# Optimization experiments

Measured on AMD Instinct MI355X. Metric: run time of the kernel, lower is better.

Reference implementation:

```python
import jax, jax.numpy as jnp
import numpy as np

N, E, C, D, H = 50000, 1600000, 50000, 128, 512


def setup_inputs() -> dict:
    key = jax.random.key(0)
    ks = jax.random.split(key, 16)
    s = jnp.float32(0.02)  # keep activations stable through 3 layers
    inp = {}
    inp["x"] = jax.random.normal(ks[0], (N, D), jnp.float32)
    inp["edge_index"] = jax.random.randint(ks[1], (2, E), 0, N)
    inp["first_edge"] = jax.random.randint(ks[2], (2,), 0, N)
    inp["candidate_edges"] = jax.random.randint(ks[3], (C, 2), 0, N)
    inp["t"] = jax.random.uniform(ks[4], (1, 1), jnp.float32)
    dims = [(D, H), (H, H), (H, H)]
    i = 5
    for l, (di, do) in enumerate(dims):
        inp[f"gin{l}_w1"] = jax.random.normal(ks[i], (di, do), jnp.float32) * s; i += 1
        inp[f"gin{l}_b1"] = jnp.zeros((do,), jnp.float32)
        inp[f"gin{l}_w2"] = jax.random.normal(ks[i], (do, do), jnp.float32) * s; i += 1
        inp[f"gin{l}_b2"] = jnp.zeros((do,), jnp.float32)
    inp["pred_w1"] = jax.random.normal(ks[i], (5 * H, H), jnp.float32) * s; i += 1
    inp["pred_b1"] = jnp.zeros((H,), jnp.float32)
    inp["pred_w2"] = jax.random.normal(ks[i], (H, 1), jnp.float32) * s; i += 1
    inp["pred_b2"] = jnp.zeros((1,), jnp.float32)
    inp["time_w1"] = jax.random.normal(ks[i], (1, H), jnp.float32) * s; i += 1
    inp["time_b1"] = jnp.zeros((H,), jnp.float32)
    inp["time_w2"] = jax.random.normal(ks[i], (H, H), jnp.float32) * s; i += 1
    inp["time_b2"] = jnp.zeros((H,), jnp.float32)
    return inp


def _edge_rep(x, u, v):
    # 'sum_absdiff': cat([x_u + x_v, |x_u - x_v|]) -> 2*H features
    xu, xv = x[u], x[v]
    return jnp.concatenate([xu + xv, jnp.abs(xu - xv)], axis=-1)


def reference(x, edge_index, first_edge, candidate_edges, t,
              gin0_w1, gin0_b1, gin0_w2, gin0_b2,
              gin1_w1, gin1_b1, gin1_w2, gin1_b2,
              gin2_w1, gin2_b1, gin2_w2, gin2_b2,
              pred_w1, pred_b1, pred_w2, pred_b2,
              time_w1, time_b1, time_w2, time_b2):
    src, dst = edge_index[0], edge_index[1]
    layers = [(gin0_w1, gin0_b1, gin0_w2, gin0_b2),
              (gin1_w1, gin1_b1, gin1_w2, gin1_b2),
              (gin2_w1, gin2_b1, gin2_w2, gin2_b2)]
    # GINConv (eps=0): h_i = MLP(x_i + sum_{j->i} x_j)
    for w1, b1, w2, b2 in layers:
        agg = jax.ops.segment_sum(x[src], dst, num_segments=x.shape[0])
        h = x + agg
        x = jax.nn.relu(h @ w1 + b1) @ w2 + b2
    first_feat = _edge_rep(x, first_edge[0], first_edge[1])  # [2H]
    t_embed = (jax.nn.relu(t @ time_w1 + time_b1) @ time_w2 + time_b2)[0]  # [H]
    cand_feat = _edge_rep(x, candidate_edges[:, 0], candidate_edges[:, 1])  # [C, 2H]
    Cn = cand_feat.shape[0]
    feat = jnp.concatenate([
        jnp.broadcast_to(first_feat, (Cn, first_feat.shape[0])),
        cand_feat,
        jnp.broadcast_to(t_embed, (Cn, t_embed.shape[0])),
    ], axis=-1)  # [C, 5H]
    logits = (jax.nn.relu(feat @ pred_w1 + pred_b1) @ pred_w2 + pred_b2)[:, 0]  # [C]
    return logits
```

## Files before the change

kernel.cpp:

```cpp
#include <hip/hip_runtime.h>

typedef __bf16 bf16x2 __attribute__((ext_vector_type(2)));
typedef __bf16 bf16x4 __attribute__((ext_vector_type(4)));
typedef __bf16 bf16x8 __attribute__((ext_vector_type(8)));
typedef float f32x4 __attribute__((ext_vector_type(4)));

#define LDSTR 40

__global__ void hist_kernel(const int* __restrict__ dst, int* __restrict__ deg, int E) {
    int i = blockIdx.x * 256 + threadIdx.x;
    if (i < E) atomicAdd(&deg[dst[i]], 1);
}

__global__ __launch_bounds__(1024)
void scan_kernel(const int* __restrict__ deg, int* __restrict__ rowptr,
                 int* __restrict__ cursor, int n) {
    __shared__ int part[1024];
    int tid = threadIdx.x;
    int chunk = (n + 1023) >> 10;
    int beg = tid * chunk;
    int fin = min(beg + chunk, n);
    int s = 0;
    for (int i = beg; i < fin; i++) s += deg[i];
    part[tid] = s;
    __syncthreads();
    for (int off = 1; off < 1024; off <<= 1) {
        int v = (tid >= off) ? part[tid - off] : 0;
        __syncthreads();
        part[tid] += v;
        __syncthreads();
    }
    int run = (tid == 0) ? 0 : part[tid - 1];
    for (int i = beg; i < fin; i++) {
        rowptr[i] = run; cursor[i] = run; run += deg[i];
    }
    if (tid == 1023) rowptr[n] = run;
}

__global__ void scatter_kernel(const int* __restrict__ src, const int* __restrict__ dst,
                               int* __restrict__ cursor, int* __restrict__ colsrc, int E) {
    int i = blockIdx.x * 256 + threadIdx.x;
    if (i < E) {
        int p = atomicAdd(&cursor[dst[i]], 1);
        colsrc[p] = src[i];
    }
}

__global__ void f32_to_bf16_kernel(const float* __restrict__ in, __bf16* __restrict__ out, int n4) {
    int i = blockIdx.x * 256 + threadIdx.x;
    if (i < n4) {
        float4 f = ((const float4*)in)[i];
        bf16x4 o;
        o[0] = (__bf16)f.x; o[1] = (__bf16)f.y; o[2] = (__bf16)f.z; o[3] = (__bf16)f.w;
        ((bf16x4*)out)[i] = o;
    }
}

__global__ void wprep_kernel(const float* __restrict__ in, __bf16* __restrict__ out, int kbits) {
    int idx = blockIdx.x * 256 + threadIdx.x;
    int K = 1 << kbits;
    if (idx < (512 << kbits)) {
        int k = idx & (K - 1);
        int n = idx >> kbits;
        out[idx] = (__bf16)in[k * 512 + n];
    }
}

template<int F>
__global__ __launch_bounds__(256)
void agg_kernel(const __bf16* __restrict__ xb, const int* __restrict__ rowptr,
                const int* __restrict__ colsrc, __bf16* __restrict__ h, int n) {
    const int node = blockIdx.x * 4 + (threadIdx.x >> 6);
    if (node >= n) return;
    const int lane = threadIdx.x & 63;
    const int DIM = F * 64;
    float acc[F];
    {
        const __bf16* p = xb + (size_t)node * DIM + lane * F;
        if constexpr (F == 8) {
            bf16x8 v = *(const bf16x8*)p;
            #pragma unroll
            for (int i = 0; i < 8; i++) acc[i] = (float)v[i];
        } else {
            bf16x2 v = *(const bf16x2*)p;
            acc[0] = (float)v[0]; acc[1] = (float)v[1];
        }
    }
    int e = rowptr[node], end = rowptr[node + 1];
    for (; e + 4 <= end; e += 4) {
        int s0 = colsrc[e], s1 = colsrc[e + 1], s2 = colsrc[e + 2], s3 = colsrc[e + 3];
        if constexpr (F == 8) {
            bf16x8 v0 = *(const bf16x8*)(xb + (size_t)s0 * DIM + lane * F);
            bf16x8 v1 = *(const bf16x8*)(xb + (size_t)s1 * DIM + lane * F);
            bf16x8 v2 = *(const bf16x8*)(xb + (size_t)s2 * DIM + lane * F);
            bf16x8 v3 = *(const bf16x8*)(xb + (size_t)s3 * DIM + lane * F);
            #pragma unroll
            for (int i = 0; i < 8; i++)
                acc[i] += ((float)v0[i] + (float)v1[i]) + ((float)v2[i] + (float)v3[i]);
        } else {
            bf16x2 v0 = *(const bf16x2*)(xb + (size_t)s0 * DIM + lane * F);
            bf16x2 v1 = *(const bf16x2*)(xb + (size_t)s1 * DIM + lane * F);
            bf16x2 v2 = *(const bf16x2*)(xb + (size_t)s2 * DIM + lane * F);
            bf16x2 v3 = *(const bf16x2*)(xb + (size_t)s3 * DIM + lane * F);
            acc[0] += ((float)v0[0] + (float)v1[0]) + ((float)v2[0] + (float)v3[0]);
            acc[1] += ((float)v0[1] + (float)v1[1]) + ((float)v2[1] + (float)v3[1]);
        }
    }
    for (; e < end; e++) {
        int s0 = colsrc[e];
        const __bf16* p0 = xb + (size_t)s0 * DIM + lane * F;
        if constexpr (F == 8) {
            bf16x8 v0 = *(const bf16x8*)p0;
            #pragma unroll
            for (int i = 0; i < 8; i++) acc[i] += (float)v0[i];
        } else {
            bf16x2 v0 = *(const bf16x2*)p0;
            acc[0] += (float)v0[0]; acc[1] += (float)v0[1];
        }
    }
    __bf16* out = h + (size_t)node * DIM + lane * F;
    if constexpr (F == 8) {
        bf16x8 o;
        #pragma unroll
        for (int i = 0; i < 8; i++) o[i] = (__bf16)acc[i];
        *(bf16x8*)out = o;
    } else {
        bf16x2 o; o[0] = (__bf16)acc[0]; o[1] = (__bf16)acc[1];
        *(bf16x2*)out = o;
    }
}

template<int AMODE, bool RELU>
__global__ __launch_bounds__(512, 2)
void gemm_kernel(const __bf16* __restrict__ A, const __bf16* __restrict__ Xb,
                 const int* __restrict__ cand, const __bf16* __restrict__ Bt,
                 const float* __restrict__ bias, __bf16* __restrict__ Cout,
                 int M, int K) {
    __shared__ __bf16 sA[64 * LDSTR];
    __shared__ __bf16 sB[512 * LDSTR];

    const int tid = threadIdx.x;
    const int lane = tid & 63;
    const int waveN = tid >> 6;
    const int mlane = lane & 15;
    const int quad = lane >> 4;
    const int rowBase = blockIdx.x * 64;

    const int ar = tid >> 3;
    const int ac = (tid & 7) << 2;
    const int br = tid >> 2;
    const int bc = (tid & 3) << 3;

    const f32x4 fzero = {0.f, 0.f, 0.f, 0.f};
    f32x4 acc[4][4];
    #pragma unroll
    for (int i = 0; i < 4; i++)
        #pragma unroll
        for (int j = 0; j < 4; j++) acc[i][j] = fzero;

    int uu = 0, vv = 0;
    const int grow = rowBase + ar;
    if (AMODE == 1 && grow < M) { uu = cand[2 * grow]; vv = cand[2 * grow + 1]; }

    for (int k0 = 0; k0 < K; k0 += 32) {
        __syncthreads();
        {
            bf16x4 av = {};
            if (AMODE == 0) {
                if (grow < M) av = *(const bf16x4*)(A + (size_t)grow * K + k0 + ac);
            } else {
                if (grow < M) {
                    int k = k0 + ac;
                    int kk = k & 511;
                    bf16x4 xu = *(const bf16x4*)(Xb + (size_t)uu * 512 + kk);
                    bf16x4 xv = *(const bf16x4*)(Xb + (size_t)vv * 512 + kk);
                    if (k < 512) {
                        #pragma unroll
                        for (int q = 0; q < 4; q++) av[q] = (__bf16)((float)xu[q] + (float)xv[q]);
                    } else {
                        #pragma unroll
                        for (int q = 0; q < 4; q++) av[q] = (__bf16)fabsf((float)xu[q] - (float)xv[q]);
                    }
                }
            }
            *(bf16x4*)(sA + ar * LDSTR + ac) = av;
        }
        #pragma unroll
        for (int i = 0; i < 4; i++) {
            int nn = br + i * 128;
            bf16x8 b = *(const bf16x8*)(Bt + (size_t)nn * K + k0 + bc);
            *(bf16x8*)(sB + nn * LDSTR + bc) = b;
        }
        __syncthreads();

        bf16x8 aF[4], bF[4];
        #pragma unroll
        for (int mt = 0; mt < 4; mt++)
            aF[mt] = *(const bf16x8*)(sA + (mt * 16 + mlane) * LDSTR + quad * 8);
        #pragma unroll
        for (int nt = 0; nt < 4; nt++)
            bF[nt] = *(const bf16x8*)(sB + (waveN * 64 + nt * 16 + mlane) * LDSTR + quad * 8);
        #pragma unroll
        for (int mt = 0; mt < 4; mt++)
            #pragma unroll
            for (int nt = 0; nt < 4; nt++)
                acc[mt][nt] = __builtin_amdgcn_mfma_f32_16x16x32_bf16(aF[mt], bF[nt], acc[mt][nt], 0, 0, 0);
    }

    #pragma unroll
    for (int mt = 0; mt < 4; mt++) {
        #pragma unroll
        for (int nt = 0; nt < 4; nt++) {
            int col = waveN * 64 + nt * 16 + mlane;
            float bv = bias[col];
            #pragma unroll
            for (int r = 0; r < 4; r++) {
                int row = rowBase + mt * 16 + quad * 4 + r;
                if (row < M) {
                    float v = acc[mt][nt][r] + bv;
                    if (RELU) v = fmaxf(v, 0.f);
                    Cout[(size_t)row * 512 + col] = (__bf16)v;
                }
            }
        }
    }
}

__global__ __launch_bounds__(512)
void constvec_kernel(const __bf16* __restrict__ xb, const int* __restrict__ first_edge,
                     const float* __restrict__ t,
                     const float* __restrict__ tw1, const float* __restrict__ tb1,
                     const float* __restrict__ tw2, const float* __restrict__ tb2,
                     const float* __restrict__ pw1, const float* __restrict__ pb1,
                     float* __restrict__ cvec) {
    __shared__ float z1[512];
    __shared__ float te[512];
    __shared__ float ff[1024];
    int tid = threadIdx.x;
    float tv = t[0];
    z1[tid] = fmaxf(tv * tw1[tid] + tb1[tid], 0.f);
    int u = first_edge[0], v = first_edge[1];
    float xu = (float)xb[(size_t)u * 512 + tid];
    float xv = (float)xb[(size_t)v * 512 + tid];
    ff[tid] = xu + xv;
    ff[512 + tid] = fabsf(xu - xv);
    __syncthreads();
    float s = tb2[tid];
    for (int j = 0; j < 512; j++) s += z1[j] * tw2[j * 512 + tid];
    te[tid] = s;
    __syncthreads();
    float c = pb1[tid];
    for (int k = 0; k < 1024; k++) c += ff[k] * pw1[k * 512 + tid];
    for (int j = 0; j < 512; j++) c += te[j] * pw1[(2048 + j) * 512 + tid];
    cvec[tid] = c;
}

__global__ __launch_bounds__(256)
void logits_kernel(const __bf16* __restrict__ Z, const float* __restrict__ w2,
                   const float* __restrict__ b2, float* __restrict__ out, int C) {
    int c = blockIdx.x * 4 + (threadIdx.x >> 6);
    if (c >= C) return;
    int lane = threadIdx.x & 63;
    bf16x8 z = *(const bf16x8*)(Z + (size_t)c * 512 + lane * 8);
    const float4* w = (const float4*)(w2 + lane * 8);
    float4 w0 = w[0], w1 = w[1];
    float s = (float)z[0] * w0.x + (float)z[1] * w0.y + (float)z[2] * w0.z + (float)z[3] * w0.w
            + (float)z[4] * w1.x + (float)z[5] * w1.y + (float)z[6] * w1.z + (float)z[7] * w1.w;
    #pragma unroll
    for (int off = 32; off > 0; off >>= 1) s += __shfl_down(s, off);
    if (lane == 0) out[c] = s + b2[0];
}

extern "C" void kernel_launch(void* const* d_in, const int* in_sizes, int n_in,
                              void* d_out, int out_size, void* d_ws, size_t ws_size,
                              hipStream_t stream) {
    (void)n_in; (void)out_size; (void)ws_size;
    const float* x          = (const float*)d_in[0];
    const int*   edge_index = (const int*)d_in[1];
    const int*   first_edge = (const int*)d_in[2];
    const int*   cand       = (const int*)d_in[3];
    const float* t          = (const float*)d_in[4];
    const float* gw1[3] = {(const float*)d_in[5], (const float*)d_in[9],  (const float*)d_in[13]};
    const float* gb1[3] = {(const float*)d_in[6], (const float*)d_in[10], (const float*)d_in[14]};
    const float* gw2[3] = {(const float*)d_in[7], (const float*)d_in[11], (const float*)d_in[15]};
    const float* gb2[3] = {(const float*)d_in[8], (const float*)d_in[12], (const float*)d_in[16]};
    const float* pw1 = (const float*)d_in[17];
    const float* pb1 = (const float*)d_in[18];
    const float* pw2 = (const float*)d_in[19];
    const float* pb2 = (const float*)d_in[20];
    const float* tw1 = (const float*)d_in[21];
    const float* tb1 = (const float*)d_in[22];
    const float* tw2 = (const float*)d_in[23];
    const float* tb2 = (const float*)d_in[24];

    const int N = in_sizes[0] / 128;
    const int E = in_sizes[1] / 2;
    const int C = in_sizes[3] / 2;

    char* p = (char*)d_ws;
    auto alloc = [&](size_t bytes) -> void* {
        void* r = (void*)p;
        p += (bytes + 255) & ~(size_t)255;
        return r;
    };
    __bf16* h    = (__bf16*)alloc((size_t)N * 512 * 2);
    __bf16* u    = (__bf16*)alloc((size_t)N * 512 * 2);
    __bf16* xb   = (__bf16*)alloc((size_t)N * 512 * 2);
    __bf16* wt01 = (__bf16*)alloc((size_t)512 * 128 * 2);
    __bf16* wt02 = (__bf16*)alloc((size_t)512 * 512 * 2);
    __bf16* wt11 = (__bf16*)alloc((size_t)512 * 512 * 2);
    __bf16* wt12 = (__bf16*)alloc((size_t)512 * 512 * 2);
    __bf16* wt21 = (__bf16*)alloc((size_t)512 * 512 * 2);
    __bf16* wt22 = (__bf16*)alloc((size_t)512 * 512 * 2);
    __bf16* wtH  = (__bf16*)alloc((size_t)512 * 1024 * 2);
    int* rowptr = (int*)alloc((size_t)(N + 1) * 4);
    int* deg    = (int*)alloc((size_t)N * 4);
    int* cursor = (int*)alloc((size_t)N * 4);
    int* colsrc = (int*)alloc((size_t)E * 4);
    float* cvec = (float*)alloc(512 * 4);
    __bf16* xb0 = (__bf16*)u;

    const int* src = edge_index;
    const int* dst = edge_index + E;

    hipMemsetAsync(deg, 0, (size_t)N * 4, stream);
    int eb = (E + 255) / 256;
    hist_kernel<<<eb, 256, 0, stream>>>(dst, deg, E);
    scan_kernel<<<1, 1024, 0, stream>>>(deg, rowptr, cursor, N);
    scatter_kernel<<<eb, 256, 0, stream>>>(src, dst, cursor, colsrc, E);

    f32_to_bf16_kernel<<<((N * 128 / 4) + 255) / 256, 256, 0, stream>>>(x, xb0, N * 128 / 4);
    wprep_kernel<<<((512 << 7)  + 255) / 256, 256, 0, stream>>>(gw1[0], wt01, 7);
    wprep_kernel<<<((512 << 9)  + 255) / 256, 256, 0, stream>>>(gw2[0], wt02, 9);
    wprep_kernel<<<((512 << 9)  + 255) / 256, 256, 0, stream>>>(gw1[1], wt11, 9);
    wprep_kernel<<<((512 << 9)  + 255) / 256, 256, 0, stream>>>(gw2[1], wt12, 9);
    wprep_kernel<<<((512 << 9)  + 255) / 256, 256, 0, stream>>>(gw1[2], wt21, 9);
    wprep_kernel<<<((512 << 9)  + 255) / 256, 256, 0, stream>>>(gw2[2], wt22, 9);
    wprep_kernel<<<((512 << 10) + 255) / 256, 256, 0, stream>>>(pw1 + (size_t)1024 * 512, wtH, 10);

    int gblocks = (N + 63) / 64;
    int ablocks = (N + 3) / 4;

    agg_kernel<2><<<ablocks, 256, 0, stream>>>(xb0, rowptr, colsrc, h, N);
    gemm_kernel<0, true ><<<gblocks, 512, 0, stream>>>(h, nullptr, nullptr, wt01, gb1[0], u,  N, 128);
    gemm_kernel<0, false><<<gblocks, 512, 0, stream>>>(u, nullptr, nullptr, wt02, gb2[0], xb, N, 512);
    agg_kernel<8><<<ablocks, 256, 0, stream>>>(xb, rowptr, colsrc, h, N);
    gemm_kernel<0, true ><<<gblocks, 512, 0, stream>>>(h, nullptr, nullptr, wt11, gb1[1], u,  N, 512);
    gemm_kernel<0, false><<<gblocks, 512, 0, stream>>>(u, nullptr, nullptr, wt12, gb2[1], xb, N, 512);
    agg_kernel<8><<<ablocks, 256, 0, stream>>>(xb, rowptr, colsrc, h, N);
    gemm_kernel<0, true ><<<gblocks, 512, 0, stream>>>(h, nullptr, nullptr, wt21, gb1[2], u,  N, 512);
    gemm_kernel<0, false><<<gblocks, 512, 0, stream>>>(u, nullptr, nullptr, wt22, gb2[2], xb, N, 512);

    constvec_kernel<<<1, 512, 0, stream>>>(xb, first_edge, t, tw1, tb1, tw2, tb2, pw1, pb1, cvec);
    int hblocks = (C + 63) / 64;
    gemm_kernel<1, true><<<hblocks, 512, 0, stream>>>(nullptr, xb, cand, wtH, cvec, u, C, 1024);
    logits_kernel<<<(C + 3) / 4, 256, 0, stream>>>(u, pw2, pb2, (float*)d_out, C);
}
```

Before: 1.482 ms.

## Split 512-wide aggregation into column slices and add nontemporal loads/stores

The 512-wide neighbor aggregation now runs as two passes, each covering a 256-column slice, so the gathered source rows per pass take half the footprint and are more likely to stay in cache. Streaming buffers (the fp32 input, the GEMM A operands, the intermediate GEMM outputs and the logits input) use nontemporal loads and stores so they do not evict the reused gather data. In exchange, the CSR index arrays are read twice, and each lane loads 8 bytes per row instead of 16.

```diff
diff --git a/kernel.cpp b/kernel.cpp
--- a/kernel.cpp
+++ b/kernel.cpp
@@ -49,9 +49,9 @@
 __global__ void f32_to_bf16_kernel(const float* __restrict__ in, __bf16* __restrict__ out, int n4) {
     int i = blockIdx.x * 256 + threadIdx.x;
     if (i < n4) {
-        float4 f = ((const float4*)in)[i];
+        f32x4 f = __builtin_nontemporal_load((const f32x4*)in + i);
         bf16x4 o;
-        o[0] = (__bf16)f.x; o[1] = (__bf16)f.y; o[2] = (__bf16)f.z; o[3] = (__bf16)f.w;
+        o[0] = (__bf16)f[0]; o[1] = (__bf16)f[1]; o[2] = (__bf16)f[2]; o[3] = (__bf16)f[3];
         ((bf16x4*)out)[i] = o;
     }
 }
@@ -66,71 +66,72 @@
     }
 }
 
-template<int F>
 __global__ __launch_bounds__(256)
-void agg_kernel(const __bf16* __restrict__ xb, const int* __restrict__ rowptr,
-                const int* __restrict__ colsrc, __bf16* __restrict__ h, int n) {
+void agg_kernel2(const __bf16* __restrict__ xb, const int* __restrict__ rowptr,
+                 const int* __restrict__ colsrc, __bf16* __restrict__ h, int n) {
     const int node = blockIdx.x * 4 + (threadIdx.x >> 6);
     if (node >= n) return;
     const int lane = threadIdx.x & 63;
-    const int DIM = F * 64;
-    float acc[F];
+    float acc[2];
     {
-        const __bf16* p = xb + (size_t)node * DIM + lane * F;
-        if constexpr (F == 8) {
-            bf16x8 v = *(const bf16x8*)p;
-            #pragma unroll
-            for (int i = 0; i < 8; i++) acc[i] = (float)v[i];
-        } else {
-            bf16x2 v = *(const bf16x2*)p;
-            acc[0] = (float)v[0]; acc[1] = (float)v[1];
-        }
+        bf16x2 v = *(const bf16x2*)(xb + (size_t)node * 128 + lane * 2);
+        acc[0] = (float)v[0]; acc[1] = (float)v[1];
     }
     int e = rowptr[node], end = rowptr[node + 1];
     for (; e + 4 <= end; e += 4) {
         int s0 = colsrc[e], s1 = colsrc[e + 1], s2 = colsrc[e + 2], s3 = colsrc[e + 3];
-        if constexpr (F == 8) {
-            bf16x8 v0 = *(const bf16x8*)(xb + (size_t)s0 * DIM + lane * F);
-            bf16x8 v1 = *(const bf16x8*)(xb + (size_t)s1 * DIM + lane * F);
-            bf16x8 v2 = *(const bf16x8*)(xb + (size_t)s2 * DIM + lane * F);
-            bf16x8 v3 = *(const bf16x8*)(xb + (size_t)s3 * DIM + lane * F);
-            #pragma unroll
-            for (int i = 0; i < 8; i++)
-                acc[i] += ((float)v0[i] + (float)v1[i]) + ((float)v2[i] + (float)v3[i]);
-        } else {
-            bf16x2 v0 = *(const bf16x2*)(xb + (size_t)s0 * DIM + lane * F);
-            bf16x2 v1 = *(const bf16x2*)(xb + (size_t)s1 * DIM + lane * F);
-            bf16x2 v2 = *(const bf16x2*)(xb + (size_t)s2 * DIM + lane * F);
-            bf16x2 v3 = *(const bf16x2*)(xb + (size_t)s3 * DIM + lane * F);
-            acc[0] += ((float)v0[0] + (float)v1[0]) + ((float)v2[0] + (float)v3[0]);
-            acc[1] += ((float)v0[1] + (float)v1[1]) + ((float)v2[1] + (float)v3[1]);
-        }
+        bf16x2 v0 = *(const bf16x2*)(xb + (size_t)s0 * 128 + lane * 2);
+        bf16x2 v1 = *(const bf16x2*)(xb + (size_t)s1 * 128 + lane * 2);
+        bf16x2 v2 = *(const bf16x2*)(xb + (size_t)s2 * 128 + lane * 2);
+        bf16x2 v3 = *(const bf16x2*)(xb + (size_t)s3 * 128 + lane * 2);
+        acc[0] += ((float)v0[0] + (float)v1[0]) + ((float)v2[0] + (float)v3[0]);
+        acc[1] += ((float)v0[1] + (float)v1[1]) + ((float)v2[1] + (float)v3[1]);
     }
     for (; e < end; e++) {
-        int s0 = colsrc[e];
-        const __bf16* p0 = xb + (size_t)s0 * DIM + lane * F;
-        if constexpr (F == 8) {
-            bf16x8 v0 = *(const bf16x8*)p0;
-            #pragma unroll
-            for (int i = 0; i < 8; i++) acc[i] += (float)v0[i];
-        } else {
-            bf16x2 v0 = *(const bf16x2*)p0;
-            acc[0] += (float)v0[0]; acc[1] += (float)v0[1];
-        }
-    }
-    __bf16* out = h + (size_t)node * DIM + lane * F;
-    if constexpr (F == 8) {
-        bf16x8 o;
-        #pragma unroll
-        for (int i = 0; i < 8; i++) o[i] = (__bf16)acc[i];
-        *(bf16x8*)out = o;
-    } else {
-        bf16x2 o; o[0] = (__bf16)acc[0]; o[1] = (__bf16)acc[1];
-        *(bf16x2*)out = o;
-    }
-}
-
-template<int AMODE, bool RELU>
+        bf16x2 v0 = *(const bf16x2*)(xb + (size_t)colsrc[e] * 128 + lane * 2);
+        acc[0] += (float)v0[0]; acc[1] += (float)v0[1];
+    }
+    bf16x2 o; o[0] = (__bf16)acc[0]; o[1] = (__bf16)acc[1];
+    __builtin_nontemporal_store(o, (bf16x2*)(h + (size_t)node * 128 + lane * 2));
+}
+
+__global__ __launch_bounds__(256)
+void agg_slice_kernel(const __bf16* __restrict__ xb, const int* __restrict__ rowptr,
+                      const int* __restrict__ colsrc, __bf16* __restrict__ h, int n,
+                      int colOff) {
+    const int node = blockIdx.x * 4 + (threadIdx.x >> 6);
+    if (node >= n) return;
+    const int lane = threadIdx.x & 63;
+    const int off = colOff + lane * 4;
+    float acc[4];
+    {
+        bf16x4 v = *(const bf16x4*)(xb + (size_t)node * 512 + off);
+        #pragma unroll
+        for (int i = 0; i < 4; i++) acc[i] = (float)v[i];
+    }
+    int e = rowptr[node], end = rowptr[node + 1];
+    for (; e + 4 <= end; e += 4) {
+        int s0 = colsrc[e], s1 = colsrc[e + 1], s2 = colsrc[e + 2], s3 = colsrc[e + 3];
+        bf16x4 v0 = *(const bf16x4*)(xb + (size_t)s0 * 512 + off);
+        bf16x4 v1 = *(const bf16x4*)(xb + (size_t)s1 * 512 + off);
+        bf16x4 v2 = *(const bf16x4*)(xb + (size_t)s2 * 512 + off);
+        bf16x4 v3 = *(const bf16x4*)(xb + (size_t)s3 * 512 + off);
+        #pragma unroll
+        for (int i = 0; i < 4; i++)
+            acc[i] += ((float)v0[i] + (float)v1[i]) + ((float)v2[i] + (float)v3[i]);
+    }
+    for (; e < end; e++) {
+        bf16x4 v0 = *(const bf16x4*)(xb + (size_t)colsrc[e] * 512 + off);
+        #pragma unroll
+        for (int i = 0; i < 4; i++) acc[i] += (float)v0[i];
+    }
+    bf16x4 o;
+    #pragma unroll
+    for (int i = 0; i < 4; i++) o[i] = (__bf16)acc[i];
+    __builtin_nontemporal_store(o, (bf16x4*)(h + (size_t)node * 512 + off));
+}
+
+template<int AMODE, bool RELU, bool NTOUT>
 __global__ __launch_bounds__(512, 2)
 void gemm_kernel(const __bf16* __restrict__ A, const __bf16* __restrict__ Xb,
                  const int* __restrict__ cand, const __bf16* __restrict__ Bt,
@@ -167,7 +168,8 @@
         {
             bf16x4 av = {};
             if (AMODE == 0) {
-                if (grow < M) av = *(const bf16x4*)(A + (size_t)grow * K + k0 + ac);
+                if (grow < M)
+                    av = __builtin_nontemporal_load((const bf16x4*)(A + (size_t)grow * K + k0 + ac));
             } else {
                 if (grow < M) {
                     int k = k0 + ac;
@@ -219,7 +221,9 @@
                 if (row < M) {
                     float v = acc[mt][nt][r] + bv;
                     if (RELU) v = fmaxf(v, 0.f);
-                    Cout[(size_t)row * 512 + col] = (__bf16)v;
+                    __bf16 ov = (__bf16)v;
+                    if (NTOUT) __builtin_nontemporal_store(ov, Cout + (size_t)row * 512 + col);
+                    else Cout[(size_t)row * 512 + col] = ov;
                 }
             }
         }
@@ -261,7 +265,7 @@
     int c = blockIdx.x * 4 + (threadIdx.x >> 6);
     if (c >= C) return;
     int lane = threadIdx.x & 63;
-    bf16x8 z = *(const bf16x8*)(Z + (size_t)c * 512 + lane * 8);
+    bf16x8 z = __builtin_nontemporal_load((const bf16x8*)(Z + (size_t)c * 512 + lane * 8));
     const float4* w = (const float4*)(w2 + lane * 8);
     float4 w0 = w[0], w1 = w[1];
     float s = (float)z[0] * w0.x + (float)z[1] * w0.y + (float)z[2] * w0.z + (float)z[3] * w0.w
@@ -323,7 +327,7 @@
     const int* src = edge_index;
     const int* dst = edge_index + E;
 
-    hipMemsetAsync(deg, 0, (size_t)N * 4, stream);
+    (void)hipMemsetAsync(deg, 0, (size_t)N * 4, stream);
     int eb = (E + 255) / 256;
     hist_kernel<<<eb, 256, 0, stream>>>(dst, deg, E);
     scan_kernel<<<1, 1024, 0, stream>>>(deg, rowptr, cursor, N);
@@ -341,18 +345,20 @@
     int gblocks = (N + 63) / 64;
     int ablocks = (N + 3) / 4;
 
-    agg_kernel<2><<<ablocks, 256, 0, stream>>>(xb0, rowptr, colsrc, h, N);
-    gemm_kernel<0, true ><<<gblocks, 512, 0, stream>>>(h, nullptr, nullptr, wt01, gb1[0], u,  N, 128);
-    gemm_kernel<0, false><<<gblocks, 512, 0, stream>>>(u, nullptr, nullptr, wt02, gb2[0], xb, N, 512);
-    agg_kernel<8><<<ablocks, 256, 0, stream>>>(xb, rowptr, colsrc, h, N);
-    gemm_kernel<0, true ><<<gblocks, 512, 0, stream>>>(h, nullptr, nullptr, wt11, gb1[1], u,  N, 512);
-    gemm_kernel<0, false><<<gblocks, 512, 0, stream>>>(u, nullptr, nullptr, wt12, gb2[1], xb, N, 512);
-    agg_kernel<8><<<ablocks, 256, 0, stream>>>(xb, rowptr, colsrc, h, N);
-    gemm_kernel<0, true ><<<gblocks, 512, 0, stream>>>(h, nullptr, nullptr, wt21, gb1[2], u,  N, 512);
-    gemm_kernel<0, false><<<gblocks, 512, 0, stream>>>(u, nullptr, nullptr, wt22, gb2[2], xb, N, 512);
+    agg_kernel2<<<ablocks, 256, 0, stream>>>(xb0, rowptr, colsrc, h, N);
+    gemm_kernel<0, true,  true ><<<gblocks, 512, 0, stream>>>(h, nullptr, nullptr, wt01, gb1[0], u,  N, 128);
+    gemm_kernel<0, false, false><<<gblocks, 512, 0, stream>>>(u, nullptr, nullptr, wt02, gb2[0], xb, N, 512);
+    agg_slice_kernel<<<ablocks, 256, 0, stream>>>(xb, rowptr, colsrc, h, N, 0);
+    agg_slice_kernel<<<ablocks, 256, 0, stream>>>(xb, rowptr, colsrc, h, N, 256);
+    gemm_kernel<0, true,  true ><<<gblocks, 512, 0, stream>>>(h, nullptr, nullptr, wt11, gb1[1], u,  N, 512);
+    gemm_kernel<0, false, false><<<gblocks, 512, 0, stream>>>(u, nullptr, nullptr, wt12, gb2[1], xb, N, 512);
+    agg_slice_kernel<<<ablocks, 256, 0, stream>>>(xb, rowptr, colsrc, h, N, 0);
+    agg_slice_kernel<<<ablocks, 256, 0, stream>>>(xb, rowptr, colsrc, h, N, 256);
+    gemm_kernel<0, true,  true ><<<gblocks, 512, 0, stream>>>(h, nullptr, nullptr, wt21, gb1[2], u,  N, 512);
+    gemm_kernel<0, false, false><<<gblocks, 512, 0, stream>>>(u, nullptr, nullptr, wt22, gb2[2], xb, N, 512);
 
     constvec_kernel<<<1, 512, 0, stream>>>(xb, first_edge, t, tw1, tb1, tw2, tb2, pw1, pb1, cvec);
     int hblocks = (C + 63) / 64;
-    gemm_kernel<1, true><<<hblocks, 512, 0, stream>>>(nullptr, xb, cand, wtH, cvec, u, C, 1024);
+    gemm_kernel<1, true, true><<<hblocks, 512, 0, stream>>>(nullptr, xb, cand, wtH, cvec, u, C, 1024);
     logits_kernel<<<(C + 3) / 4, 256, 0, stream>>>(u, pw2, pb2, (float*)d_out, C);
 }
```

Result: slower. 1.662 ms (+12.1%).

## Retile GEMM to 128x128 blocks with direct global-to-LDS loads

Applied to the files above, without the earlier changes.

The GEMM kernel is rebuilt around 128x128 output tiles split over a 2D grid with 256 threads and four waves in a 2x2 layout, replacing 64x512 tiles with 512 threads. A and B tiles are now copied straight from global memory into LDS with global_load_lds, so they no longer pass through registers. The old padded LDS stride is dropped and unpadded 32-wide rows are used, which may cause bank conflicts. The aim is better occupancy and more A reuse per block, at the cost of reading each A row-tile four times across the N-blocks. The conversion kernel also switches to nontemporal loads.

```diff
diff --git a/kernel.cpp b/kernel.cpp
--- a/kernel.cpp
+++ b/kernel.cpp
@@ -1,11 +1,17 @@
 #include <hip/hip_runtime.h>
+#include <stdint.h>
 
 typedef __bf16 bf16x2 __attribute__((ext_vector_type(2)));
 typedef __bf16 bf16x4 __attribute__((ext_vector_type(4)));
 typedef __bf16 bf16x8 __attribute__((ext_vector_type(8)));
 typedef float f32x4 __attribute__((ext_vector_type(4)));
 
-#define LDSTR 40
+typedef __attribute__((address_space(3))) uint8_t lds_u8;
+typedef const __attribute__((address_space(1))) uint8_t g_u8;
+
+static __device__ __forceinline__ void gload_lds16(const void* g, void* l) {
+    __builtin_amdgcn_global_load_lds((g_u8*)g, (lds_u8*)l, 16, 0, 0);
+}
 
 __global__ void hist_kernel(const int* __restrict__ dst, int* __restrict__ deg, int E) {
     int i = blockIdx.x * 256 + threadIdx.x;
@@ -49,9 +55,9 @@
 __global__ void f32_to_bf16_kernel(const float* __restrict__ in, __bf16* __restrict__ out, int n4) {
     int i = blockIdx.x * 256 + threadIdx.x;
     if (i < n4) {
-        float4 f = ((const float4*)in)[i];
+        f32x4 f = __builtin_nontemporal_load((const f32x4*)in + i);
         bf16x4 o;
-        o[0] = (__bf16)f.x; o[1] = (__bf16)f.y; o[2] = (__bf16)f.z; o[3] = (__bf16)f.w;
+        o[0] = (__bf16)f[0]; o[1] = (__bf16)f[1]; o[2] = (__bf16)f[2]; o[3] = (__bf16)f[3];
         ((bf16x4*)out)[i] = o;
     }
 }
@@ -107,8 +113,7 @@
         }
     }
     for (; e < end; e++) {
-        int s0 = colsrc[e];
-        const __bf16* p0 = xb + (size_t)s0 * DIM + lane * F;
+        const __bf16* p0 = xb + (size_t)colsrc[e] * DIM + lane * F;
         if constexpr (F == 8) {
             bf16x8 v0 = *(const bf16x8*)p0;
             #pragma unroll
@@ -131,25 +136,23 @@
 }
 
 template<int AMODE, bool RELU>
-__global__ __launch_bounds__(512, 2)
+__global__ __launch_bounds__(256, 3)
 void gemm_kernel(const __bf16* __restrict__ A, const __bf16* __restrict__ Xb,
                  const int* __restrict__ cand, const __bf16* __restrict__ Bt,
                  const float* __restrict__ bias, __bf16* __restrict__ Cout,
                  int M, int K) {
-    __shared__ __bf16 sA[64 * LDSTR];
-    __shared__ __bf16 sB[512 * LDSTR];
+    __shared__ __bf16 sA[128 * 32];
+    __shared__ __bf16 sB[128 * 32];
 
     const int tid = threadIdx.x;
     const int lane = tid & 63;
-    const int waveN = tid >> 6;
+    const int wid = tid >> 6;
+    const int waveM = wid & 1;
+    const int waveN = wid >> 1;
     const int mlane = lane & 15;
     const int quad = lane >> 4;
-    const int rowBase = blockIdx.x * 64;
-
-    const int ar = tid >> 3;
-    const int ac = (tid & 7) << 2;
-    const int br = tid >> 2;
-    const int bc = (tid & 3) << 3;
+    const int rowBase = blockIdx.x * 128;
+    const int nBase = blockIdx.y * 128;
 
     const f32x4 fzero = {0.f, 0.f, 0.f, 0.f};
     f32x4 acc[4][4];
@@ -158,48 +161,65 @@
         #pragma unroll
         for (int j = 0; j < 4; j++) acc[i][j] = fzero;
 
+    const int srow = lane >> 2;
+    const int scol = (lane & 3) << 3;
+
     int uu = 0, vv = 0;
-    const int grow = rowBase + ar;
-    if (AMODE == 1 && grow < M) { uu = cand[2 * grow]; vv = cand[2 * grow + 1]; }
+    const int c_row = tid >> 1;
+    const int c_col = (tid & 1) << 4;
+    if (AMODE == 1) {
+        int gr = min(rowBase + c_row, M - 1);
+        uu = cand[2 * gr]; vv = cand[2 * gr + 1];
+    }
 
     for (int k0 = 0; k0 < K; k0 += 32) {
         __syncthreads();
-        {
-            bf16x4 av = {};
-            if (AMODE == 0) {
-                if (grow < M) av = *(const bf16x4*)(A + (size_t)grow * K + k0 + ac);
+        if (AMODE == 0) {
+            #pragma unroll
+            for (int j = 0; j < 2; j++) {
+                int c = wid * 2 + j;
+                int grow = min(rowBase + 16 * c + srow, M - 1);
+                gload_lds16(A + (size_t)grow * K + k0 + scol, sA + c * 512);
+            }
+        } else {
+            int k = k0 + c_col;
+            int kk = k & 511;
+            bf16x8 xu0 = *(const bf16x8*)(Xb + (size_t)uu * 512 + kk);
+            bf16x8 xu1 = *(const bf16x8*)(Xb + (size_t)uu * 512 + kk + 8);
+            bf16x8 xv0 = *(const bf16x8*)(Xb + (size_t)vv * 512 + kk);
+            bf16x8 xv1 = *(const bf16x8*)(Xb + (size_t)vv * 512 + kk + 8);
+            bf16x8 a0, a1;
+            if (k < 512) {
+                #pragma unroll
+                for (int q = 0; q < 8; q++) {
+                    a0[q] = (__bf16)((float)xu0[q] + (float)xv0[q]);
+                    a1[q] = (__bf16)((float)xu1[q] + (float)xv1[q]);
+                }
             } else {
-                if (grow < M) {
-                    int k = k0 + ac;
-                    int kk = k & 511;
-                    bf16x4 xu = *(const bf16x4*)(Xb + (size_t)uu * 512 + kk);
-                    bf16x4 xv = *(const bf16x4*)(Xb + (size_t)vv * 512 + kk);
-                    if (k < 512) {
-                        #pragma unroll
-                        for (int q = 0; q < 4; q++) av[q] = (__bf16)((float)xu[q] + (float)xv[q]);
-                    } else {
-                        #pragma unroll
-                        for (int q = 0; q < 4; q++) av[q] = (__bf16)fabsf((float)xu[q] - (float)xv[q]);
-                    }
+                #pragma unroll
+                for (int q = 0; q < 8; q++) {
+                    a0[q] = (__bf16)fabsf((float)xu0[q] - (float)xv0[q]);
+                    a1[q] = (__bf16)fabsf((float)xu1[q] - (float)xv1[q]);
                 }
             }
-            *(bf16x4*)(sA + ar * LDSTR + ac) = av;
-        }
-        #pragma unroll
-        for (int i = 0; i < 4; i++) {
-            int nn = br + i * 128;
-            bf16x8 b = *(const bf16x8*)(Bt + (size_t)nn * K + k0 + bc);
-            *(bf16x8*)(sB + nn * LDSTR + bc) = b;
+            *(bf16x8*)(sA + c_row * 32 + c_col) = a0;
+            *(bf16x8*)(sA + c_row * 32 + c_col + 8) = a1;
+        }
+        #pragma unroll
+        for (int j = 0; j < 2; j++) {
+            int c = wid * 2 + j;
+            int nrow = nBase + 16 * c + srow;
+            gload_lds16(Bt + (size_t)nrow * K + k0 + scol, sB + c * 512);
         }
         __syncthreads();
 
         bf16x8 aF[4], bF[4];
         #pragma unroll
         for (int mt = 0; mt < 4; mt++)
-            aF[mt] = *(const bf16x8*)(sA + (mt * 16 + mlane) * LDSTR + quad * 8);
+            aF[mt] = *(const bf16x8*)(sA + (waveM * 64 + mt * 16 + mlane) * 32 + quad * 8);
         #pragma unroll
         for (int nt = 0; nt < 4; nt++)
-            bF[nt] = *(const bf16x8*)(sB + (waveN * 64 + nt * 16 + mlane) * LDSTR + quad * 8);
+            bF[nt] = *(const bf16x8*)(sB + (waveN * 64 + nt * 16 + mlane) * 32 + quad * 8);
         #pragma unroll
         for (int mt = 0; mt < 4; mt++)
             #pragma unroll
@@ -211,11 +231,11 @@
     for (int mt = 0; mt < 4; mt++) {
         #pragma unroll
         for (int nt = 0; nt < 4; nt++) {
-            int col = waveN * 64 + nt * 16 + mlane;
+            int col = nBase + waveN * 64 + nt * 16 + mlane;
             float bv = bias[col];
             #pragma unroll
             for (int r = 0; r < 4; r++) {
-                int row = rowBase + mt * 16 + quad * 4 + r;
+                int row = rowBase + waveM * 64 + mt * 16 + quad * 4 + r;
                 if (row < M) {
                     float v = acc[mt][nt][r] + bv;
                     if (RELU) v = fmaxf(v, 0.f);
@@ -323,7 +343,7 @@
     const int* src = edge_index;
     const int* dst = edge_index + E;
 
-    hipMemsetAsync(deg, 0, (size_t)N * 4, stream);
+    (void)hipMemsetAsync(deg, 0, (size_t)N * 4, stream);
     int eb = (E + 255) / 256;
     hist_kernel<<<eb, 256, 0, stream>>>(dst, deg, E);
     scan_kernel<<<1, 1024, 0, stream>>>(deg, rowptr, cursor, N);
@@ -338,21 +358,21 @@
     wprep_kernel<<<((512 << 9)  + 255) / 256, 256, 0, stream>>>(gw2[2], wt22, 9);
     wprep_kernel<<<((512 << 10) + 255) / 256, 256, 0, stream>>>(pw1 + (size_t)1024 * 512, wtH, 10);
 
-    int gblocks = (N + 63) / 64;
+    dim3 ggrid((N + 127) / 128, 4);
     int ablocks = (N + 3) / 4;
 
     agg_kernel<2><<<ablocks, 256, 0, stream>>>(xb0, rowptr, colsrc, h, N);
-    gemm_kernel<0, true ><<<gblocks, 512, 0, stream>>>(h, nullptr, nullptr, wt01, gb1[0], u,  N, 128);
-    gemm_kernel<0, false><<<gblocks, 512, 0, stream>>>(u, nullptr, nullptr, wt02, gb2[0], xb, N, 512);
+    gemm_kernel<0, true ><<<ggrid, 256, 0, stream>>>(h, nullptr, nullptr, wt01, gb1[0], u,  N, 128);
+    gemm_kernel<0, false><<<ggrid, 256, 0, stream>>>(u, nullptr, nullptr, wt02, gb2[0], xb, N, 512);
     agg_kernel<8><<<ablocks, 256, 0, stream>>>(xb, rowptr, colsrc, h, N);
-    gemm_kernel<0, true ><<<gblocks, 512, 0, stream>>>(h, nullptr, nullptr, wt11, gb1[1], u,  N, 512);
-    gemm_kernel<0, false><<<gblocks, 512, 0, stream>>>(u, nullptr, nullptr, wt12, gb2[1], xb, N, 512);
+    gemm_kernel<0, true ><<<ggrid, 256, 0, stream>>>(h, nullptr, nullptr, wt11, gb1[1], u,  N, 512);
+    gemm_kernel<0, false><<<ggrid, 256, 0, stream>>>(u, nullptr, nullptr, wt12, gb2[1], xb, N, 512);
     agg_kernel<8><<<ablocks, 256, 0, stream>>>(xb, rowptr, colsrc, h, N);
-    gemm_kernel<0, true ><<<gblocks, 512, 0, stream>>>(h, nullptr, nullptr, wt21, gb1[2], u,  N, 512);
-    gemm_kernel<0, false><<<gblocks, 512, 0, stream>>>(u, nullptr, nullptr, wt22, gb2[2], xb, N, 512);
+    gemm_kernel<0, true ><<<ggrid, 256, 0, stream>>>(h, nullptr, nullptr, wt21, gb1[2], u,  N, 512);
+    gemm_kernel<0, false><<<ggrid, 256, 0, stream>>>(u, nullptr, nullptr, wt22, gb2[2], xb, N, 512);
 
     constvec_kernel<<<1, 512, 0, stream>>>(xb, first_edge, t, tw1, tb1, tw2, tb2, pw1, pb1, cvec);
-    int hblocks = (C + 63) / 64;
-    gemm_kernel<1, true><<<hblocks, 512, 0, stream>>>(nullptr, xb, cand, wtH, cvec, u, C, 1024);
+    dim3 hgrid((C + 127) / 128, 4);
+    gemm_kernel<1, true><<<hgrid, 256, 0, stream>>>(nullptr, xb, cand, wtH, cvec, u, C, 1024);
     logits_kernel<<<(C + 3) / 4, 256, 0, stream>>>(u, pw2, pb2, (float*)d_out, C);
 }
```

Result: slower. 1.524 ms (+2.8%).
